# Performance work log

Measured on AMD Instinct MI355X. Metric: run time of the kernel, lower is better.

Reference implementation:

```python
import jax, jax.numpy as jnp
import numpy as np
from jax import lax

K = 3
PAD = 1

def setup_inputs() -> dict:
    key = jax.random.key(0)
    ks = jax.random.split(key, 5)
    B, C, H, W, O = 4, 128, 128, 128, 256
    x = jax.random.normal(ks[0], (B, C, H, W), dtype=jnp.float32)
    w_off = jax.random.normal(ks[1], (3 * K * K, C, K, K), dtype=jnp.float32) * 0.05
    b_off = jnp.zeros((3 * K * K,), dtype=jnp.float32)
    w_dw = jax.random.normal(ks[2], (C, 1, K, K), dtype=jnp.float32) * 0.2
    b_dw = jnp.zeros((C,), dtype=jnp.float32)
    w_pw = jax.random.normal(ks[3], (O, C), dtype=jnp.float32) * (1.0 / np.sqrt(C))
    b_pw = jnp.zeros((O,), dtype=jnp.float32)
    return {"x": x, "w_off": w_off, "b_off": b_off, "w_dw": w_dw,
            "b_dw": b_dw, "w_pw": w_pw, "b_pw": b_pw}

def _dcn_forward(x, w_off, b_off, w_dw, b_dw, w_pw, b_pw):
    B, C, H, W = x.shape
    K2 = K * K
    # offset/mask conv (stride 1, pad 1) -> [B, 3*K*K, H, W]
    om = lax.conv_general_dilated(
        x, w_off, window_strides=(1, 1), padding=[(PAD, PAD), (PAD, PAD)],
        dimension_numbers=("NCHW", "OIHW", "NCHW")) + b_off[None, :, None, None]
    off = om[:, : 2 * K2]                      # [B, 2*K2, H, W]
    mask = jax.nn.sigmoid(om[:, 2 * K2:])      # [B, K2, H, W]
    dy = off[:, 0::2]                          # [B, K2, H, W] (y offsets)
    dx = off[:, 1::2]                          # [B, K2, H, W] (x offsets)
    # base sampling grid per kernel tap
    ky, kx = jnp.meshgrid(jnp.arange(K), jnp.arange(K), indexing="ij")
    ky = (ky.reshape(-1) - PAD).astype(x.dtype)   # [K2]
    kx = (kx.reshape(-1) - PAD).astype(x.dtype)
    py = jnp.arange(H, dtype=x.dtype)[None, None, :, None] + ky[None, :, None, None] + dy
    px = jnp.arange(W, dtype=x.dtype)[None, None, None, :] + kx[None, :, None, None] + dx
    y0 = jnp.floor(py); x0 = jnp.floor(px)
    wy = py - y0;       wx = px - x0

    def gather(yc, xc):
        # yc, xc: [B, K2, H, W] float corner coords; zero outside bounds
        valid = ((yc >= 0) & (yc < H) & (xc >= 0) & (xc < W)).astype(x.dtype)
        yi = jnp.clip(yc, 0, H - 1).astype(jnp.int32)
        xi = jnp.clip(xc, 0, W - 1).astype(jnp.int32)
        idx = yi * W + xi                       # [B, K2, H, W]
        def per_b(xb, ib):
            # xb: [C, H, W]; ib: [K2, H, W] -> [C, K2, H, W]
            return jnp.take(xb.reshape(C, -1), ib.reshape(-1), axis=1).reshape(C, K2, H, W)
        v = jax.vmap(per_b)(x, idx)             # [B, C, K2, H, W]
        return v * valid[:, None]

    val = (gather(y0, x0) * ((1 - wy) * (1 - wx))[:, None]
           + gather(y0, x0 + 1) * ((1 - wy) * wx)[:, None]
           + gather(y0 + 1, x0) * (wy * (1 - wx))[:, None]
           + gather(y0 + 1, x0 + 1) * (wy * wx)[:, None])  # [B, C, K2, H, W]
    val = val * mask[:, None]
    # depthwise deformable conv: per-channel K2 weights
    wk = w_dw.reshape(C, K2)
    out = jnp.einsum("bckhw,ck->bchw", val, wk) + b_dw[None, :, None, None]
    # pointwise 1x1 conv
    out = jnp.einsum("bchw,oc->bohw", out, w_pw) + b_pw[None, :, None, None]
    return out

def reference(x, w_off, b_off, w_dw, b_dw, w_pw, b_pw):
    return _dcn_forward(x, w_off, b_off, w_dw, b_dw, w_pw, b_pw)
```

## Files before the change

### kernel.cpp

```cpp
#include <hip/hip_runtime.h>
#include <hip/hip_bf16.h>
#include <math.h>

#define BB 4
#define CC 128
#define HH 128
#define WW 128
#define OO 256
#define HWP 16384

typedef __attribute__((ext_vector_type(8))) _Float16 half8;
typedef __attribute__((ext_vector_type(2))) _Float16 half2t;
typedef __attribute__((ext_vector_type(4))) float floatx4;

__device__ inline half2t u2h2(unsigned int u) {
  union { unsigned int i; half2t h; } z; z.i = u; return z.h;
}
__device__ inline unsigned short f2h_bits(float f) {
  union { _Float16 h; unsigned short s; } z; z.h = (_Float16)f; return z.s;
}

__device__ inline void blend2(unsigned int a00w, unsigned int a01w,
                              unsigned int a10w, unsigned int a11w,
                              half2t wt, half2t wb, float wk0, float wk1,
                              float& acc0, float& acc1) {
  unsigned int tl = __builtin_amdgcn_perm(a01w, a00w, 0x05040100u);
  unsigned int th = __builtin_amdgcn_perm(a01w, a00w, 0x07060302u);
  unsigned int bl = __builtin_amdgcn_perm(a11w, a10w, 0x05040100u);
  unsigned int bh = __builtin_amdgcn_perm(a11w, a10w, 0x07060302u);
  float v0 = __builtin_amdgcn_fdot2(u2h2(bl), wb, __builtin_amdgcn_fdot2(u2h2(tl), wt, 0.f, false), false);
  float v1 = __builtin_amdgcn_fdot2(u2h2(bh), wb, __builtin_amdgcn_fdot2(u2h2(th), wt, 0.f, false), false);
  acc0 = fmaf(v0, wk0, acc0);
  acc1 = fmaf(v1, wk1, acc1);
}

__global__ __launch_bounds__(256) void k_transpose(const float* __restrict__ x,
                                                   const float* __restrict__ w_off,
                                                   const float* __restrict__ w_pw,
                                                   unsigned int* __restrict__ xh32,
                                                   _Float16* __restrict__ Ah,
                                                   _Float16* __restrict__ Apw) {
  int tid = threadIdx.x;
  if (blockIdx.z == 4) {
    int e = (blockIdx.x * 128 + blockIdx.y) * 256 + tid;
    if (e < 144 * 32 * 8) {
      int kblk = e >> 8;
      int o = (e >> 3) & 31;
      int j = e & 7;
      int k = kblk * 8 + j;
      int t = k >> 7, c = k & 127;
      float w = (o < 27) ? w_off[(o * CC + c) * 9 + t] : 0.0f;
      Ah[e] = (_Float16)w;
    }
    int e2 = e - 144 * 32 * 8;
    if (e2 >= 0 && e2 < 16 * 256 * 8) {
      int cblk = e2 >> 11;
      int o = (e2 >> 3) & 255;
      int j = e2 & 7;
      Apw[e2] = (_Float16)w_pw[o * CC + cblk * 8 + j];
    }
    return;
  }
  __shared__ float tile[64][65];
  int wt = blockIdx.x & 1;
  int ct = blockIdx.x >> 1;
  int h = blockIdx.y, b = blockIdx.z;
  int tw = tid & 63;
  int tc = tid >> 6;
#pragma unroll
  for (int i = 0; i < 16; i++) {
    int c = ct * 64 + i * 4 + tc;
    tile[i * 4 + tc][tw] = x[((b * CC + c) * HH + h) * WW + wt * 64 + tw];
  }
  __syncthreads();
  int cp = tid & 31;
  int wq = tid >> 5;
#pragma unroll
  for (int i = 0; i < 8; i++) {
    int wp = i * 8 + wq;
    int w = wt * 64 + wp;
    unsigned short h0 = f2h_bits(tile[cp * 2][wp]);
    unsigned short h1 = f2h_bits(tile[cp * 2 + 1][wp]);
    int idx2 = (((b * HH + h) * WW + w) * CC + ct * 64 + cp * 2) >> 1;
    xh32[idx2] = (unsigned int)h0 | ((unsigned int)h1 << 16);
  }
}

__global__ __launch_bounds__(256, 2) void k_fused(
    const _Float16* __restrict__ xh, const _Float16* __restrict__ Ah,
    const _Float16* __restrict__ Apw, const float* __restrict__ b_off,
    const float* __restrict__ w_dw, const float* __restrict__ b_dw,
    const float* __restrict__ bpw, float* __restrict__ out) {
  __shared__ float om_s[64][28];
  __shared__ int s_base[64][9];
  __shared__ int s_dxs[64][9];
  __shared__ int s_dys[64][9];
  __shared__ unsigned int s_wp[64][9][2];
  __shared__ float s_wk[9][128];
  __shared__ __align__(16) _Float16 val[64][128];

  int tid = threadIdx.x;
  int bid = blockIdx.x;
  int n0 = ((bid & 7) * 128 + (bid >> 3)) * 64;
  int b = n0 >> 14;
  int h0 = (n0 >> 7) & 127;
  int wbase = n0 & 127;

  int wv = tid >> 6, lane = tid & 63;
  int n16 = lane & 15, quad = lane >> 4;

  {
    int pxb = wv * 16;
    floatx4 acc0 = {}, acc1 = {};
    half8 zz = {};
#pragma unroll
    for (int t = 0; t < 9; t++) {
      int dy = t / 3 - 1, dx = t % 3 - 1;
      int hs = h0 + dy;
      bool hok = ((unsigned)hs < HH);
      int hsc = min(max(hs, 0), HH - 1);
      int wA = wbase + pxb + n16 + dx;
      bool okA = hok && ((unsigned)wA < WW);
      int wAc = min(max(wA, 0), WW - 1);
      size_t rowoff = (size_t)((b * HH + hsc) * WW + wAc) * CC + quad * 8;
#pragma unroll
      for (int cs = 0; cs < 4; cs++) {
        half8 bh = *(const half8*)(xh + rowoff + cs * 32);
        bh = okA ? bh : zz;
        int kblk = t * 16 + cs * 4 + quad;
        const _Float16* pa = Ah + (size_t)kblk * 256 + n16 * 8;
        half8 a0 = *(const half8*)pa;
        half8 a1 = *(const half8*)(pa + 128);
        acc0 = __builtin_amdgcn_mfma_f32_16x16x32_f16(a0, bh, acc0, 0, 0, 0);
        acc1 = __builtin_amdgcn_mfma_f32_16x16x32_f16(a1, bh, acc1, 0, 0, 0);
      }
    }
    int px = pxb + n16;
#pragma unroll
    for (int reg = 0; reg < 4; reg++) {
      int o0 = quad * 4 + reg;
      om_s[px][o0] = acc0[reg] + b_off[o0];
      int o1 = 16 + quad * 4 + reg;
      if (o1 < 27) om_s[px][o1] = acc1[reg] + b_off[o1];
    }
  }
  __syncthreads();

  for (int i = tid; i < 1152; i += 256) s_wk[i % 9][i / 9] = w_dw[i];
  for (int it = tid; it < 576; it += 256) {
    int px = it / 9, k = it - px * 9;
    int w = wbase + px;
    float dyv = om_s[px][2 * k];
    float dxv = om_s[px][2 * k + 1];
    float mv = om_s[px][18 + k];
    mv = 1.0f / (1.0f + __expf(-mv));
    float py = (float)(h0 + k / 3 - 1) + dyv;
    float pxf = (float)(w + k % 3 - 1) + dxv;
    float y0f = floorf(py), x0f = floorf(pxf);
    float wy = py - y0f, wx = pxf - x0f;
    int y0 = (int)y0f, x0 = (int)x0f;
    int y1 = y0 + 1, x1 = x0 + 1;
    float v00 = (y0 >= 0 && y0 < HH && x0 >= 0 && x0 < WW) ? 1.f : 0.f;
    float v01 = (y0 >= 0 && y0 < HH && x1 >= 0 && x1 < WW) ? 1.f : 0.f;
    float v10 = (y1 >= 0 && y1 < HH && x0 >= 0 && x0 < WW) ? 1.f : 0.f;
    float v11 = (y1 >= 0 && y1 < HH && x1 >= 0 && x1 < WW) ? 1.f : 0.f;
    int y0c = min(max(y0, 0), HH - 1), y1c = min(max(y1, 0), HH - 1);
    int x0c = min(max(x0, 0), WW - 1), x1c = min(max(x1, 0), WW - 1);
    s_base[px][k] = ((b * HH + y0c) * WW + x0c) * CC;
    s_dxs[px][k] = (x1c - x0c) * CC;
    s_dys[px][k] = (y1c - y0c) * WW * CC;
    float w00 = (1.f - wy) * (1.f - wx) * mv * v00;
    float w01 = (1.f - wy) * wx * mv * v01;
    float w10 = wy * (1.f - wx) * mv * v10;
    float w11 = wy * wx * mv * v11;
    s_wp[px][k][0] = (unsigned int)f2h_bits(w00) | ((unsigned int)f2h_bits(w01) << 16);
    s_wp[px][k][1] = (unsigned int)f2h_bits(w10) | ((unsigned int)f2h_bits(w11) << 16);
  }
  __syncthreads();

  {
    int cl = lane & 15;
    int pgl = lane >> 4;
    int slot = wv * 4 + pgl;
    int c0 = cl * 8;
    const unsigned short* xs = (const unsigned short*)xh;

    float ac[4][8];
#pragma unroll
    for (int p = 0; p < 4; p++)
#pragma unroll
      for (int j = 0; j < 8; j++) ac[p][j] = 0.f;

#pragma unroll
    for (int k = 0; k < 9; k++) {
      float4 wka = *(const float4*)&s_wk[k][c0];
      float4 wkb = *(const float4*)&s_wk[k][c0 + 4];
#pragma unroll
      for (int p = 0; p < 4; p++) {
        int pix = slot + p * 16;
        int base = s_base[pix][k] + c0;
        int dxs = s_dxs[pix][k], dys = s_dys[pix][k];
        uint4 a00 = *(const uint4*)(xs + base);
        uint4 a01 = *(const uint4*)(xs + base + dxs);
        uint4 a10 = *(const uint4*)(xs + base + dys);
        uint4 a11 = *(const uint4*)(xs + base + dys + dxs);
        half2t wt = u2h2(s_wp[pix][k][0]);
        half2t wb = u2h2(s_wp[pix][k][1]);
        blend2(a00.x, a01.x, a10.x, a11.x, wt, wb, wka.x, wka.y, ac[p][0], ac[p][1]);
        blend2(a00.y, a01.y, a10.y, a11.y, wt, wb, wka.z, wka.w, ac[p][2], ac[p][3]);
        blend2(a00.z, a01.z, a10.z, a11.z, wt, wb, wkb.x, wkb.y, ac[p][4], ac[p][5]);
        blend2(a00.w, a01.w, a10.w, a11.w, wt, wb, wkb.z, wkb.w, ac[p][6], ac[p][7]);
      }
    }
    float4 bd0 = *(const float4*)(b_dw + c0);
    float4 bd1 = *(const float4*)(b_dw + c0 + 4);
#pragma unroll
    for (int p = 0; p < 4; p++) {
      int pix = slot + p * 16;
      uint4 pk;
      pk.x = (unsigned int)f2h_bits(ac[p][0] + bd0.x) | ((unsigned int)f2h_bits(ac[p][1] + bd0.y) << 16);
      pk.y = (unsigned int)f2h_bits(ac[p][2] + bd0.z) | ((unsigned int)f2h_bits(ac[p][3] + bd0.w) << 16);
      pk.z = (unsigned int)f2h_bits(ac[p][4] + bd1.x) | ((unsigned int)f2h_bits(ac[p][5] + bd1.y) << 16);
      pk.w = (unsigned int)f2h_bits(ac[p][6] + bd1.z) | ((unsigned int)f2h_bits(ac[p][7] + bd1.w) << 16);
      int su = cl ^ (pix & 7);
      *(uint4*)&val[pix][su * 8] = pk;
    }
  }
  __syncthreads();

  {
    int obase = wv * 64;
    floatx4 acc[4][4] = {};
#pragma unroll
    for (int cs = 0; cs < 4; cs++) {
      half8 af[4], bf[4];
#pragma unroll
      for (int mf = 0; mf < 4; mf++) {
        const _Float16* pa = Apw + ((size_t)(cs * 4 + quad) * 256 + obase + mf * 16 + n16) * 8;
        af[mf] = *(const half8*)pa;
      }
#pragma unroll
      for (int nf = 0; nf < 4; nf++) {
        int row = nf * 16 + n16;
        int su = (cs * 4 + quad) ^ (row & 7);
        bf[nf] = *(const half8*)&val[row][su * 8];
      }
#pragma unroll
      for (int mf = 0; mf < 4; mf++)
#pragma unroll
        for (int nf = 0; nf < 4; nf++)
          acc[mf][nf] = __builtin_amdgcn_mfma_f32_16x16x32_f16(af[mf], bf[nf], acc[mf][nf], 0, 0, 0);
    }
#pragma unroll
    for (int mf = 0; mf < 4; mf++) {
#pragma unroll
      for (int reg = 0; reg < 4; reg++) {
        int o = obase + mf * 16 + quad * 4 + reg;
        float bo = bpw[o];
#pragma unroll
        for (int nf = 0; nf < 4; nf++) {
          int n = n0 + nf * 16 + n16;
          int hw = n & 16383;
          out[((size_t)(b * OO + o) << 14) + hw] = acc[mf][nf][reg] + bo;
        }
      }
    }
  }
}

extern "C" void kernel_launch(void* const* d_in, const int* in_sizes, int n_in,
                              void* d_out, int out_size, void* d_ws, size_t ws_size,
                              hipStream_t stream) {
  const float* x     = (const float*)d_in[0];
  const float* w_off = (const float*)d_in[1];
  const float* b_off = (const float*)d_in[2];
  const float* w_dw  = (const float*)d_in[3];
  const float* b_dw  = (const float*)d_in[4];
  const float* w_pw  = (const float*)d_in[5];
  const float* b_pw  = (const float*)d_in[6];
  float* out = (float*)d_out;
  float* ws  = (float*)d_ws;

  _Float16* xh  = (_Float16*)ws;
  _Float16* Ah  = (_Float16*)((char*)ws + 16777216);
  _Float16* Apw = Ah + 36864;

  k_transpose<<<dim3(4, 128, 5), 256, 0, stream>>>(x, w_off, w_pw,
                                                   (unsigned int*)xh, Ah, Apw);
  k_fused<<<1024, 256, 0, stream>>>(xh, Ah, Apw, b_off, w_dw, b_dw, b_pw, out);
}
```

Before: 161.3 us.

## Restructure deformable gather per-wave with pipelined loads and higher occupancy

The transpose kernel is rewritten to use float4 loads and uint4 stores over 32-channel tiles. In the fused kernel, each wave now computes offsets only for its own 16 pixels, which removes two block barriers. The gather is remapped so each lane owns two channels per pixel, with double-buffered register loads of the four bilinear corners. Corner addresses are packed into one int with flag bits and read via readfirstlane, depthwise weights are held in registers, and om_s is swizzled. Launch bounds go to 4 blocks per CU, the pointwise GEMM is split into two halves to cut register pressure, and setprio is wrapped around the MFMAs; the trade-off is more, smaller 4-byte gather loads and possible spills.

After: 161.9 us. Within noise of the previous version (+0.3%).

```diff
diff --git a/kernel.cpp b/kernel.cpp
--- a/kernel.cpp
+++ b/kernel.cpp
@@ -32,6 +32,10 @@
   float v1 = __builtin_amdgcn_fdot2(u2h2(bh), wb, __builtin_amdgcn_fdot2(u2h2(th), wt, 0.f, false), false);
   acc0 = fmaf(v0, wk0, acc0);
   acc1 = fmaf(v1, wk1, acc1);
+}
+
+__device__ inline int om_idx(int px, int o) {
+  return (((o >> 2) ^ (px & 7)) << 2) | (o & 3);
 }
 
 __global__ __launch_bounds__(256) void k_transpose(const float* __restrict__ x,
@@ -61,42 +65,40 @@
     }
     return;
   }
-  __shared__ float tile[64][65];
-  int wt = blockIdx.x & 1;
-  int ct = blockIdx.x >> 1;
+  __shared__ float tile[32][132];
+  int ct = blockIdx.x;
   int h = blockIdx.y, b = blockIdx.z;
-  int tw = tid & 63;
-  int tc = tid >> 6;
-#pragma unroll
-  for (int i = 0; i < 16; i++) {
-    int c = ct * 64 + i * 4 + tc;
-    tile[i * 4 + tc][tw] = x[((b * CC + c) * HH + h) * WW + wt * 64 + tw];
+  int f4 = tid & 31;
+  int cl = tid >> 5;
+#pragma unroll
+  for (int i = 0; i < 4; i++) {
+    int c = cl + i * 8;
+    float4 v = *(const float4*)(x + ((size_t)(b * CC + ct * 32 + c) * HH + h) * WW + f4 * 4);
+    *(float4*)&tile[c][f4 * 4] = v;
   }
   __syncthreads();
-  int cp = tid & 31;
-  int wq = tid >> 5;
-#pragma unroll
-  for (int i = 0; i < 8; i++) {
-    int wp = i * 8 + wq;
-    int w = wt * 64 + wp;
-    unsigned short h0 = f2h_bits(tile[cp * 2][wp]);
-    unsigned short h1 = f2h_bits(tile[cp * 2 + 1][wp]);
-    int idx2 = (((b * HH + h) * WW + w) * CC + ct * 64 + cp * 2) >> 1;
-    xh32[idx2] = (unsigned int)h0 | ((unsigned int)h1 << 16);
-  }
-}
-
-__global__ __launch_bounds__(256, 2) void k_fused(
+  int cg = tid & 3;
+#pragma unroll
+  for (int pass = 0; pass < 2; pass++) {
+    int px = pass * 64 + (tid >> 2);
+    unsigned int d0, d1, d2, d3;
+    d0 = (unsigned int)f2h_bits(tile[cg * 8 + 0][px]) | ((unsigned int)f2h_bits(tile[cg * 8 + 1][px]) << 16);
+    d1 = (unsigned int)f2h_bits(tile[cg * 8 + 2][px]) | ((unsigned int)f2h_bits(tile[cg * 8 + 3][px]) << 16);
+    d2 = (unsigned int)f2h_bits(tile[cg * 8 + 4][px]) | ((unsigned int)f2h_bits(tile[cg * 8 + 5][px]) << 16);
+    d3 = (unsigned int)f2h_bits(tile[cg * 8 + 6][px]) | ((unsigned int)f2h_bits(tile[cg * 8 + 7][px]) << 16);
+    uint4 z; z.x = d0; z.y = d1; z.z = d2; z.w = d3;
+    *(uint4*)(xh32 + (size_t)((b * HH + h) * WW + px) * 64 + ct * 16 + cg * 4) = z;
+  }
+}
+
+__global__ __launch_bounds__(256, 4) void k_fused(
     const _Float16* __restrict__ xh, const _Float16* __restrict__ Ah,
     const _Float16* __restrict__ Apw, const float* __restrict__ b_off,
     const float* __restrict__ w_dw, const float* __restrict__ b_dw,
     const float* __restrict__ bpw, float* __restrict__ out) {
-  __shared__ float om_s[64][28];
-  __shared__ int s_base[64][9];
-  __shared__ int s_dxs[64][9];
-  __shared__ int s_dys[64][9];
+  __shared__ float om_s[64][32];
+  __shared__ int s_packed[64][9];
   __shared__ unsigned int s_wp[64][9][2];
-  __shared__ float s_wk[9][128];
   __shared__ __align__(16) _Float16 val[64][128];
 
   int tid = threadIdx.x;
@@ -131,137 +133,154 @@
         const _Float16* pa = Ah + (size_t)kblk * 256 + n16 * 8;
         half8 a0 = *(const half8*)pa;
         half8 a1 = *(const half8*)(pa + 128);
+        __builtin_amdgcn_s_setprio(1);
         acc0 = __builtin_amdgcn_mfma_f32_16x16x32_f16(a0, bh, acc0, 0, 0, 0);
         acc1 = __builtin_amdgcn_mfma_f32_16x16x32_f16(a1, bh, acc1, 0, 0, 0);
+        __builtin_amdgcn_s_setprio(0);
       }
     }
     int px = pxb + n16;
 #pragma unroll
     for (int reg = 0; reg < 4; reg++) {
       int o0 = quad * 4 + reg;
-      om_s[px][o0] = acc0[reg] + b_off[o0];
+      om_s[px][om_idx(px, o0)] = acc0[reg] + b_off[o0];
       int o1 = 16 + quad * 4 + reg;
-      if (o1 < 27) om_s[px][o1] = acc1[reg] + b_off[o1];
-    }
-  }
-  __syncthreads();
-
-  for (int i = tid; i < 1152; i += 256) s_wk[i % 9][i / 9] = w_dw[i];
-  for (int it = tid; it < 576; it += 256) {
-    int px = it / 9, k = it - px * 9;
-    int w = wbase + px;
-    float dyv = om_s[px][2 * k];
-    float dxv = om_s[px][2 * k + 1];
-    float mv = om_s[px][18 + k];
-    mv = 1.0f / (1.0f + __expf(-mv));
-    float py = (float)(h0 + k / 3 - 1) + dyv;
-    float pxf = (float)(w + k % 3 - 1) + dxv;
-    float y0f = floorf(py), x0f = floorf(pxf);
-    float wy = py - y0f, wx = pxf - x0f;
-    int y0 = (int)y0f, x0 = (int)x0f;
-    int y1 = y0 + 1, x1 = x0 + 1;
-    float v00 = (y0 >= 0 && y0 < HH && x0 >= 0 && x0 < WW) ? 1.f : 0.f;
-    float v01 = (y0 >= 0 && y0 < HH && x1 >= 0 && x1 < WW) ? 1.f : 0.f;
-    float v10 = (y1 >= 0 && y1 < HH && x0 >= 0 && x0 < WW) ? 1.f : 0.f;
-    float v11 = (y1 >= 0 && y1 < HH && x1 >= 0 && x1 < WW) ? 1.f : 0.f;
-    int y0c = min(max(y0, 0), HH - 1), y1c = min(max(y1, 0), HH - 1);
-    int x0c = min(max(x0, 0), WW - 1), x1c = min(max(x1, 0), WW - 1);
-    s_base[px][k] = ((b * HH + y0c) * WW + x0c) * CC;
-    s_dxs[px][k] = (x1c - x0c) * CC;
-    s_dys[px][k] = (y1c - y0c) * WW * CC;
-    float w00 = (1.f - wy) * (1.f - wx) * mv * v00;
-    float w01 = (1.f - wy) * wx * mv * v01;
-    float w10 = wy * (1.f - wx) * mv * v10;
-    float w11 = wy * wx * mv * v11;
-    s_wp[px][k][0] = (unsigned int)f2h_bits(w00) | ((unsigned int)f2h_bits(w01) << 16);
-    s_wp[px][k][1] = (unsigned int)f2h_bits(w10) | ((unsigned int)f2h_bits(w11) << 16);
-  }
-  __syncthreads();
+      if (o1 < 27) om_s[px][om_idx(px, o1)] = acc1[reg] + b_off[o1];
+    }
+  }
+
+#pragma unroll
+  for (int pass = 0; pass < 3; pass++) {
+    int it = pass * 64 + lane;
+    if (it < 144) {
+      int pxl = it / 9;
+      int k = it - pxl * 9;
+      int px = wv * 16 + pxl;
+      int w = wbase + px;
+      float dyv = om_s[px][om_idx(px, 2 * k)];
+      float dxv = om_s[px][om_idx(px, 2 * k + 1)];
+      float mvv = om_s[px][om_idx(px, 18 + k)];
+      mvv = 1.0f / (1.0f + __expf(-mvv));
+      float py = (float)(h0 + k / 3 - 1) + dyv;
+      float pxf = (float)(w + k % 3 - 1) + dxv;
+      float y0f = floorf(py), x0f = floorf(pxf);
+      float wy = py - y0f, wx = pxf - x0f;
+      int y0 = (int)y0f, x0 = (int)x0f;
+      int y1 = y0 + 1, x1 = x0 + 1;
+      float v00 = (y0 >= 0 && y0 < HH && x0 >= 0 && x0 < WW) ? 1.f : 0.f;
+      float v01 = (y0 >= 0 && y0 < HH && x1 >= 0 && x1 < WW) ? 1.f : 0.f;
+      float v10 = (y1 >= 0 && y1 < HH && x0 >= 0 && x0 < WW) ? 1.f : 0.f;
+      float v11 = (y1 >= 0 && y1 < HH && x1 >= 0 && x1 < WW) ? 1.f : 0.f;
+      int y0c = min(max(y0, 0), HH - 1), y1c = min(max(y1, 0), HH - 1);
+      int x0c = min(max(x0, 0), WW - 1), x1c = min(max(x1, 0), WW - 1);
+      int base = ((b * HH + y0c) * WW + x0c) * CC;
+      int dxf = (x1c > x0c) ? 1 : 0;
+      int dyf = (y1c > y0c) ? 1 : 0;
+      s_packed[px][k] = base | (dxf << 30) | (dyf << 31);
+      float w00 = (1.f - wy) * (1.f - wx) * mvv * v00;
+      float w01 = (1.f - wy) * wx * mvv * v01;
+      float w10 = wy * (1.f - wx) * mvv * v10;
+      float w11 = wy * wx * mvv * v11;
+      s_wp[px][k][0] = (unsigned int)f2h_bits(w00) | ((unsigned int)f2h_bits(w01) << 16);
+      s_wp[px][k][1] = (unsigned int)f2h_bits(w10) | ((unsigned int)f2h_bits(w11) << 16);
+    }
+  }
 
   {
-    int cl = lane & 15;
-    int pgl = lane >> 4;
-    int slot = wv * 4 + pgl;
-    int c0 = cl * 8;
+    int c0 = lane * 2;
     const unsigned short* xs = (const unsigned short*)xh;
-
-    float ac[4][8];
-#pragma unroll
-    for (int p = 0; p < 4; p++)
-#pragma unroll
-      for (int j = 0; j < 8; j++) ac[p][j] = 0.f;
-
-#pragma unroll
-    for (int k = 0; k < 9; k++) {
-      float4 wka = *(const float4*)&s_wk[k][c0];
-      float4 wkb = *(const float4*)&s_wk[k][c0 + 4];
-#pragma unroll
-      for (int p = 0; p < 4; p++) {
-        int pix = slot + p * 16;
-        int base = s_base[pix][k] + c0;
-        int dxs = s_dxs[pix][k], dys = s_dys[pix][k];
-        uint4 a00 = *(const uint4*)(xs + base);
-        uint4 a01 = *(const uint4*)(xs + base + dxs);
-        uint4 a10 = *(const uint4*)(xs + base + dys);
-        uint4 a11 = *(const uint4*)(xs + base + dys + dxs);
-        half2t wt = u2h2(s_wp[pix][k][0]);
-        half2t wb = u2h2(s_wp[pix][k][1]);
-        blend2(a00.x, a01.x, a10.x, a11.x, wt, wb, wka.x, wka.y, ac[p][0], ac[p][1]);
-        blend2(a00.y, a01.y, a10.y, a11.y, wt, wb, wka.z, wka.w, ac[p][2], ac[p][3]);
-        blend2(a00.z, a01.z, a10.z, a11.z, wt, wb, wkb.x, wkb.y, ac[p][4], ac[p][5]);
-        blend2(a00.w, a01.w, a10.w, a11.w, wt, wb, wkb.z, wkb.w, ac[p][6], ac[p][7]);
-      }
-    }
-    float4 bd0 = *(const float4*)(b_dw + c0);
-    float4 bd1 = *(const float4*)(b_dw + c0 + 4);
-#pragma unroll
-    for (int p = 0; p < 4; p++) {
-      int pix = slot + p * 16;
-      uint4 pk;
-      pk.x = (unsigned int)f2h_bits(ac[p][0] + bd0.x) | ((unsigned int)f2h_bits(ac[p][1] + bd0.y) << 16);
-      pk.y = (unsigned int)f2h_bits(ac[p][2] + bd0.z) | ((unsigned int)f2h_bits(ac[p][3] + bd0.w) << 16);
-      pk.z = (unsigned int)f2h_bits(ac[p][4] + bd1.x) | ((unsigned int)f2h_bits(ac[p][5] + bd1.y) << 16);
-      pk.w = (unsigned int)f2h_bits(ac[p][6] + bd1.z) | ((unsigned int)f2h_bits(ac[p][7] + bd1.w) << 16);
-      int su = cl ^ (pix & 7);
-      *(uint4*)&val[pix][su * 8] = pk;
+    float wk0[9], wk1[9];
+    {
+      const float* wp_ = w_dw + c0 * 9;
+#pragma unroll
+      for (int k = 0; k < 9; k++) { wk0[k] = wp_[k]; wk1[k] = wp_[9 + k]; }
+    }
+    float2 bdp = *(const float2*)(b_dw + c0);
+
+    unsigned int A00[9], A01[9], A10[9], A11[9];
+    unsigned int B00[9], B01[9], B10[9], B11[9];
+
+    auto issue = [&](int pxl, unsigned int* c00, unsigned int* c01,
+                     unsigned int* c10, unsigned int* c11) {
+      int px = wv * 16 + pxl;
+#pragma unroll
+      for (int k = 0; k < 9; k++) {
+        int pk = __builtin_amdgcn_readfirstlane(s_packed[px][k]);
+        int base = (pk & 0x3FFFFFFF) + c0;
+        int dxs = (pk & 0x40000000) ? CC : 0;
+        int dys = (pk & 0x80000000u) ? (WW * CC) : 0;
+        c00[k] = *(const unsigned int*)(xs + base);
+        c01[k] = *(const unsigned int*)(xs + base + dxs);
+        c10[k] = *(const unsigned int*)(xs + base + dys);
+        c11[k] = *(const unsigned int*)(xs + base + dys + dxs);
+      }
+    };
+    auto compute = [&](int pxl, const unsigned int* c00, const unsigned int* c01,
+                       const unsigned int* c10, const unsigned int* c11) {
+      int px = wv * 16 + pxl;
+      float a0 = 0.f, a1 = 0.f;
+#pragma unroll
+      for (int k = 0; k < 9; k++) {
+        uint2 w2 = *(const uint2*)&s_wp[px][k][0];
+        blend2(c00[k], c01[k], c10[k], c11[k], u2h2(w2.x), u2h2(w2.y),
+               wk0[k], wk1[k], a0, a1);
+      }
+      unsigned int d = (unsigned int)f2h_bits(a0 + bdp.x) |
+                       ((unsigned int)f2h_bits(a1 + bdp.y) << 16);
+      int su = (lane >> 2) ^ (px & 7);
+      *(unsigned int*)((char*)&val[px][0] + su * 16 + (lane & 3) * 4) = d;
+    };
+
+    issue(0, A00, A01, A10, A11);
+#pragma unroll
+    for (int i = 0; i < 16; i += 2) {
+      issue(i + 1, B00, B01, B10, B11);
+      compute(i, A00, A01, A10, A11);
+      if (i + 2 < 16) issue(i + 2, A00, A01, A10, A11);
+      compute(i + 1, B00, B01, B10, B11);
     }
   }
   __syncthreads();
 
   {
     int obase = wv * 64;
-    floatx4 acc[4][4] = {};
-#pragma unroll
-    for (int cs = 0; cs < 4; cs++) {
-      half8 af[4], bf[4];
-#pragma unroll
-      for (int mf = 0; mf < 4; mf++) {
-        const _Float16* pa = Apw + ((size_t)(cs * 4 + quad) * 256 + obase + mf * 16 + n16) * 8;
-        af[mf] = *(const half8*)pa;
-      }
-#pragma unroll
-      for (int nf = 0; nf < 4; nf++) {
-        int row = nf * 16 + n16;
-        int su = (cs * 4 + quad) ^ (row & 7);
-        bf[nf] = *(const half8*)&val[row][su * 8];
-      }
-#pragma unroll
-      for (int mf = 0; mf < 4; mf++)
-#pragma unroll
-        for (int nf = 0; nf < 4; nf++)
-          acc[mf][nf] = __builtin_amdgcn_mfma_f32_16x16x32_f16(af[mf], bf[nf], acc[mf][nf], 0, 0, 0);
-    }
-#pragma unroll
-    for (int mf = 0; mf < 4; mf++) {
-#pragma unroll
-      for (int reg = 0; reg < 4; reg++) {
-        int o = obase + mf * 16 + quad * 4 + reg;
-        float bo = bpw[o];
+#pragma unroll
+    for (int mh = 0; mh < 2; mh++) {
+      floatx4 acc[2][4] = {};
+#pragma unroll
+      for (int cs = 0; cs < 4; cs++) {
+        half8 af[2], bf[4];
+#pragma unroll
+        for (int mf = 0; mf < 2; mf++) {
+          const _Float16* pa = Apw + ((size_t)(cs * 4 + quad) * 256 + obase + (mh * 2 + mf) * 16 + n16) * 8;
+          af[mf] = *(const half8*)pa;
+        }
 #pragma unroll
         for (int nf = 0; nf < 4; nf++) {
-          int n = n0 + nf * 16 + n16;
-          int hw = n & 16383;
-          out[((size_t)(b * OO + o) << 14) + hw] = acc[mf][nf][reg] + bo;
+          int row = nf * 16 + n16;
+          int su = (cs * 4 + quad) ^ (row & 7);
+          bf[nf] = *(const half8*)&val[row][su * 8];
+        }
+        __builtin_amdgcn_s_setprio(1);
+#pragma unroll
+        for (int mf = 0; mf < 2; mf++)
+#pragma unroll
+          for (int nf = 0; nf < 4; nf++)
+            acc[mf][nf] = __builtin_amdgcn_mfma_f32_16x16x32_f16(af[mf], bf[nf], acc[mf][nf], 0, 0, 0);
+        __builtin_amdgcn_s_setprio(0);
+      }
+#pragma unroll
+      for (int mf = 0; mf < 2; mf++) {
+#pragma unroll
+        for (int reg = 0; reg < 4; reg++) {
+          int o = obase + (mh * 2 + mf) * 16 + quad * 4 + reg;
+          float bo = bpw[o];
+#pragma unroll
+          for (int nf = 0; nf < 4; nf++) {
+            int n = n0 + nf * 16 + n16;
+            int hw = n & 16383;
+            out[((size_t)(b * OO + o) << 14) + hw] = acc[mf][nf][reg] + bo;
+          }
         }
       }
     }
```
